# Performance work log

Hardware: AMD Instinct MI355X
Metric: run time of the kernel (lower is better)

Reference implementation:

```python
import jax, jax.numpy as jnp
import numpy as np

T, B, IN, H, OUT = 16384, 1, 32, 512, 1


def setup_inputs() -> dict:
    key = jax.random.key(0)
    ks = jax.random.split(key, 7)
    s = 0.05
    return {
        "input_seq": jax.random.normal(ks[0], (T, B, IN), dtype=jnp.float32),
        "W_ih": jax.random.normal(ks[1], (4 * H, IN), dtype=jnp.float32) * s,
        "W_hh": jax.random.normal(ks[2], (4 * H, H), dtype=jnp.float32) * s,
        "b_ih": jax.random.normal(ks[3], (4 * H,), dtype=jnp.float32) * s,
        "b_hh": jax.random.normal(ks[4], (4 * H,), dtype=jnp.float32) * s,
        "W_lin": jax.random.normal(ks[5], (OUT, H), dtype=jnp.float32) * s,
        "b_lin": jax.random.normal(ks[6], (OUT,), dtype=jnp.float32) * s,
    }


def reference(input_seq, W_ih, W_hh, b_ih, b_hh, W_lin, b_lin):
    # input_seq: [T, 1, IN]; batch=1 as hardcoded by the module's hidden_cell.
    t = input_seq.shape[0]
    x = input_seq.reshape(t, -1)  # [T, IN]
    h_dim = W_hh.shape[1]
    # Precompute input contribution to gates for all timesteps (one big GEMM).
    x_gates = x @ W_ih.T + (b_ih + b_hh)  # [T, 4H]

    def step(carry, xg):
        h, c = carry
        g = xg + W_hh @ h  # [4H]; PyTorch gate order: i, f, g, o
        i = jax.nn.sigmoid(g[:h_dim])
        f = jax.nn.sigmoid(g[h_dim:2 * h_dim])
        gg = jnp.tanh(g[2 * h_dim:3 * h_dim])
        o = jax.nn.sigmoid(g[3 * h_dim:])
        c_new = f * c + i * gg
        h_new = o * jnp.tanh(c_new)
        return (h_new, c_new), h_new

    h0 = jnp.zeros((h_dim,), dtype=input_seq.dtype)
    c0 = jnp.zeros((h_dim,), dtype=input_seq.dtype)
    _, lstm_out = jax.lax.scan(step, (h0, c0), x_gates)  # [T, H]
    predictions = lstm_out @ W_lin.T + b_lin  # [T, OUT]
    return predictions[-1]  # [OUT]
```

## Files before the change

### kernel.cpp

```cpp
#include <hip/hip_runtime.h>
#include <hip/hip_fp16.h>
#include <math.h>


#define T_STEPS 16384
#define IN_DIM  32
#define H_DIM   512
#define SLOTS   32
#define H_SLICE 16
#define KTOT    544
#define CHUNK   136

typedef unsigned int uint32x4 __attribute__((ext_vector_type(4)));

__device__ __forceinline__ float fast_sigmoid(float v) {
  return 1.0f / (1.0f + __expf(-v));
}
__device__ __forceinline__ float fast_tanh(float v) {
  return 2.0f / (1.0f + __expf(-2.0f * v)) - 1.0f;
}

__device__ __forceinline__ void store_pkt(unsigned int* p, unsigned int v) {
  asm volatile("global_store_dword %0, %1, off sc0 sc1"
               :: "v"(p), "v"(v) : "memory");
}
__device__ __forceinline__ uint32x4 load_pkt4(const unsigned int* p) {
  uint32x4 r;
  asm volatile("global_load_dwordx4 %0, %1, off sc0 sc1\n\ts_waitcnt vmcnt(0)"
               : "=&v"(r) : "v"(p) : "memory");
  return r;
}

__launch_bounds__(256, 1)
__global__ void lstm_scan_kernel(
    const float* __restrict__ x,
    const float* __restrict__ Wih,
    const float* __restrict__ Whh,
    const float* __restrict__ bih,
    const float* __restrict__ bhh,
    const float* __restrict__ Wlin,
    const float* __restrict__ blin,
    float* __restrict__ out,
    unsigned int* pub)
{
  const int slot = blockIdx.x;
  const int tid  = threadIdx.x;
  const int w    = tid >> 6;
  const int l    = tid & 63;

  __shared__ __align__(16) float hshm[KTOT];
  __shared__ float red[256];

  const int R = (l >> 4) * H_DIM + slot * H_SLICE + (l & 15);

  float wreg[CHUNK];
  #pragma unroll
  for (int j = 0; j < CHUNK; ++j) {
    const int k = w * CHUNK + j;
    wreg[j] = (k < H_DIM) ? Whh[R * H_DIM + k]
                          : Wih[R * IN_DIM + (k - H_DIM)];
  }
  #pragma unroll
  for (int j = 0; j < CHUNK; ++j)
    asm volatile("v_mov_b32 %0, %0" : "+v"(wreg[j]));

  const float bias = (w == 0) ? (bih[R] + bhh[R]) : 0.0f;

  float c = 0.0f;

  const bool poller = (tid < 128) && ((tid >> 2) != slot);
  if (tid < H_SLICE) hshm[slot * H_SLICE + tid] = 0.0f;

  for (int t = 0; t < T_STEPS; ++t) {
    float xv = (tid < IN_DIM) ? x[t * IN_DIM + tid] : 0.0f;

    if (poller) {
      const unsigned int* p = pub + (t & 1) * H_DIM + tid * 4;
      const unsigned int tg = (unsigned int)t & 0xFFFFu;
      uint32x4 r;
      for (;;) {
        r = load_pkt4(p);
        if ((r.x >> 16) == tg && (r.y >> 16) == tg &&
            (r.z >> 16) == tg && (r.w >> 16) == tg) break;
      }
      float4 hv4;
      hv4.x = __half2float(__ushort_as_half((unsigned short)(r.x & 0xFFFFu)));
      hv4.y = __half2float(__ushort_as_half((unsigned short)(r.y & 0xFFFFu)));
      hv4.z = __half2float(__ushort_as_half((unsigned short)(r.z & 0xFFFFu)));
      hv4.w = __half2float(__ushort_as_half((unsigned short)(r.w & 0xFFFFu)));
      *(float4*)(hshm + tid * 4) = hv4;
    }
    if (tid < IN_DIM) hshm[H_DIM + tid] = xv;
    __syncthreads();

    const float4* hv = (const float4*)(hshm + w * CHUNK);
    float a0 = 0.f, a1 = 0.f, a2 = 0.f, a3 = 0.f;
    #pragma unroll
    for (int q = 0; q < CHUNK / 4; ++q) {
      const float4 h4 = hv[q];
      a0 = fmaf(wreg[4 * q + 0], h4.x, a0);
      a1 = fmaf(wreg[4 * q + 1], h4.y, a1);
      a2 = fmaf(wreg[4 * q + 2], h4.z, a2);
      a3 = fmaf(wreg[4 * q + 3], h4.w, a3);
    }
    red[w * 64 + l] = (a0 + a1) + (a2 + a3);
    __syncthreads();

    if (w == 0) {
      const float g = bias + red[l] + red[64 + l] + red[128 + l] + red[192 + l];
      const float act = (l < 32 || l >= 48) ? fast_sigmoid(g) : fast_tanh(g);
      const int j = l & 15;
      const float ig = __shfl(act, j, 64);
      const float fg = __shfl(act, j + 16, 64);
      const float gt = __shfl(act, j + 32, 64);
      const float og = __shfl(act, j + 48, 64);
      if (l < H_SLICE) {
        c = fg * c + ig * gt;
        const float h = og * fast_tanh(c);
        hshm[slot * H_SLICE + l] = h;
        const unsigned int pkt =
            (((unsigned int)(t + 1) & 0xFFFFu) << 16) |
            (unsigned int)__half_as_ushort(__float2half_rn(h));
        store_pkt(pub + ((t + 1) & 1) * H_DIM + slot * H_SLICE + l, pkt);
      }
    }
  }

  if (slot == 0) {
    if (poller) {
      const unsigned int* p = pub + (T_STEPS & 1) * H_DIM + tid * 4;
      const unsigned int tg = (unsigned int)T_STEPS & 0xFFFFu;
      uint32x4 r;
      for (;;) {
        r = load_pkt4(p);
        if ((r.x >> 16) == tg && (r.y >> 16) == tg &&
            (r.z >> 16) == tg && (r.w >> 16) == tg) break;
      }
      float4 hv4;
      hv4.x = __half2float(__ushort_as_half((unsigned short)(r.x & 0xFFFFu)));
      hv4.y = __half2float(__ushort_as_half((unsigned short)(r.y & 0xFFFFu)));
      hv4.z = __half2float(__ushort_as_half((unsigned short)(r.z & 0xFFFFu)));
      hv4.w = __half2float(__ushort_as_half((unsigned short)(r.w & 0xFFFFu)));
      *(float4*)(hshm + tid * 4) = hv4;
    }
    __syncthreads();
    red[tid] = hshm[2 * tid] * Wlin[2 * tid] +
               hshm[2 * tid + 1] * Wlin[2 * tid + 1];
    __syncthreads();
    if (w == 0) {
      float s = red[l] + red[64 + l] + red[128 + l] + red[192 + l];
      #pragma unroll
      for (int off = 32; off > 0; off >>= 1) s += __shfl_down(s, off, 64);
      if (l == 0) out[0] = s + blin[0];
    }
  }
}

extern "C" void kernel_launch(void* const* d_in, const int* in_sizes, int n_in,
                              void* d_out, int out_size, void* d_ws, size_t ws_size,
                              hipStream_t stream) {
  const float* x    = (const float*)d_in[0];
  const float* Wih  = (const float*)d_in[1];
  const float* Whh  = (const float*)d_in[2];
  const float* bih  = (const float*)d_in[3];
  const float* bhh  = (const float*)d_in[4];
  const float* Wlin = (const float*)d_in[5];
  const float* blin = (const float*)d_in[6];
  float* out = (float*)d_out;

  unsigned int* pub = (unsigned int*)d_ws;

  hipMemsetAsync(d_ws, 0, 4096, stream);
  hipLaunchKernelGGL(lstm_scan_kernel, dim3(SLOTS), dim3(256), 0, stream,
                     x, Wih, Whh, bih, bhh, Wlin, blin, out, pub);
}
```

Measured before the change: 28.60 ms.

## Assign one gate per wave and reduce K-partials with cross-lane shuffles

Each of the four waves now owns one LSTM gate for the block's 16 hidden units. Lanes within a wave split the 544-long K dimension into quarters and combine their partials with xor shuffles, instead of writing every partial to shared memory for wave 0 to sum. All waves then apply their gate activation in parallel and exchange results through a small shared buffer. Every wave updates the cell state redundantly, and the global packet stores are spread across waves. The intent is to shorten the serial reduce-and-activate tail of each timestep, at the cost of duplicated cell arithmetic and more shuffle instructions.

```diff
diff --git a/kernel.cpp b/kernel.cpp
--- a/kernel.cpp
+++ b/kernel.cpp
@@ -9,9 +9,9 @@
 #define SLOTS   32
 #define H_SLICE 16
 #define KTOT    544
-#define CHUNK   136
+#define QCHUNK  136
 
-typedef unsigned int uint32x4 __attribute__((ext_vector_type(4)));
+typedef unsigned int uint4v __attribute__((ext_vector_type(4)));
 
 __device__ __forceinline__ float fast_sigmoid(float v) {
   return 1.0f / (1.0f + __expf(-v));
@@ -24,11 +24,15 @@
   asm volatile("global_store_dword %0, %1, off sc0 sc1"
                :: "v"(p), "v"(v) : "memory");
 }
-__device__ __forceinline__ uint32x4 load_pkt4(const unsigned int* p) {
-  uint32x4 r;
+__device__ __forceinline__ uint4v load_pkt4(const unsigned int* p) {
+  uint4v r;
   asm volatile("global_load_dwordx4 %0, %1, off sc0 sc1\n\ts_waitcnt vmcnt(0)"
                : "=&v"(r) : "v"(p) : "memory");
   return r;
+}
+
+__device__ __forceinline__ float h16(unsigned int lo16) {
+  return __half2float(__ushort_as_half((unsigned short)(lo16 & 0xFFFFu)));
 }
 
 __launch_bounds__(256, 1)
@@ -47,24 +51,27 @@
   const int tid  = threadIdx.x;
   const int w    = tid >> 6;
   const int l    = tid & 63;
+  const int q    = l >> 4;
+  const int j    = l & 15;
 
   __shared__ __align__(16) float hshm[KTOT];
+  __shared__ __align__(16) float actsh[64];
   __shared__ float red[256];
 
-  const int R = (l >> 4) * H_DIM + slot * H_SLICE + (l & 15);
+  const int R = w * H_DIM + slot * H_SLICE + j;
 
-  float wreg[CHUNK];
+  float wreg[QCHUNK];
   #pragma unroll
-  for (int j = 0; j < CHUNK; ++j) {
-    const int k = w * CHUNK + j;
-    wreg[j] = (k < H_DIM) ? Whh[R * H_DIM + k]
+  for (int i = 0; i < QCHUNK; ++i) {
+    const int k = q * QCHUNK + i;
+    wreg[i] = (k < H_DIM) ? Whh[R * H_DIM + k]
                           : Wih[R * IN_DIM + (k - H_DIM)];
   }
   #pragma unroll
-  for (int j = 0; j < CHUNK; ++j)
-    asm volatile("v_mov_b32 %0, %0" : "+v"(wreg[j]));
+  for (int i = 0; i < QCHUNK; ++i)
+    asm volatile("v_mov_b32 %0, %0" : "+v"(wreg[i]));
 
-  const float bias = (w == 0) ? (bih[R] + bhh[R]) : 0.0f;
+  const float bias = bih[R] + bhh[R];
 
   float c = 0.0f;
 
@@ -76,50 +83,46 @@
 
     if (poller) {
       const unsigned int* p = pub + (t & 1) * H_DIM + tid * 4;
-      const unsigned int tg = (unsigned int)t & 0xFFFFu;
-      uint32x4 r;
+      const unsigned int tg = (unsigned int)t;
+      uint4v r;
       for (;;) {
         r = load_pkt4(p);
         if ((r.x >> 16) == tg && (r.y >> 16) == tg &&
             (r.z >> 16) == tg && (r.w >> 16) == tg) break;
       }
       float4 hv4;
-      hv4.x = __half2float(__ushort_as_half((unsigned short)(r.x & 0xFFFFu)));
-      hv4.y = __half2float(__ushort_as_half((unsigned short)(r.y & 0xFFFFu)));
-      hv4.z = __half2float(__ushort_as_half((unsigned short)(r.z & 0xFFFFu)));
-      hv4.w = __half2float(__ushort_as_half((unsigned short)(r.w & 0xFFFFu)));
+      hv4.x = h16(r.x); hv4.y = h16(r.y); hv4.z = h16(r.z); hv4.w = h16(r.w);
       *(float4*)(hshm + tid * 4) = hv4;
     }
     if (tid < IN_DIM) hshm[H_DIM + tid] = xv;
     __syncthreads();
 
-    const float4* hv = (const float4*)(hshm + w * CHUNK);
+    const float4* hv = (const float4*)(hshm + q * QCHUNK);
     float a0 = 0.f, a1 = 0.f, a2 = 0.f, a3 = 0.f;
     #pragma unroll
-    for (int q = 0; q < CHUNK / 4; ++q) {
-      const float4 h4 = hv[q];
-      a0 = fmaf(wreg[4 * q + 0], h4.x, a0);
-      a1 = fmaf(wreg[4 * q + 1], h4.y, a1);
-      a2 = fmaf(wreg[4 * q + 2], h4.z, a2);
-      a3 = fmaf(wreg[4 * q + 3], h4.w, a3);
+    for (int i = 0; i < QCHUNK / 4; ++i) {
+      const float4 h4 = hv[i];
+      a0 = fmaf(wreg[4 * i + 0], h4.x, a0);
+      a1 = fmaf(wreg[4 * i + 1], h4.y, a1);
+      a2 = fmaf(wreg[4 * i + 2], h4.z, a2);
+      a3 = fmaf(wreg[4 * i + 3], h4.w, a3);
     }
-    red[w * 64 + l] = (a0 + a1) + (a2 + a3);
+    float acc = (a0 + a1) + (a2 + a3);
+    acc += __shfl_xor(acc, 16, 64);
+    acc += __shfl_xor(acc, 32, 64);
+    const float g = acc + bias;
+    const float act = (w == 2) ? fast_tanh(g) : fast_sigmoid(g);
+    if (l < 16) actsh[l * 4 + w] = act;
     __syncthreads();
 
-    if (w == 0) {
-      const float g = bias + red[l] + red[64 + l] + red[128 + l] + red[192 + l];
-      const float act = (l < 32 || l >= 48) ? fast_sigmoid(g) : fast_tanh(g);
-      const int j = l & 15;
-      const float ig = __shfl(act, j, 64);
-      const float fg = __shfl(act, j + 16, 64);
-      const float gt = __shfl(act, j + 32, 64);
-      const float og = __shfl(act, j + 48, 64);
-      if (l < H_SLICE) {
-        c = fg * c + ig * gt;
-        const float h = og * fast_tanh(c);
-        hshm[slot * H_SLICE + l] = h;
+    if (l < 16) {
+      const float4 a4 = *(const float4*)(actsh + l * 4);
+      c = a4.y * c + a4.x * a4.z;
+      const float h = a4.w * fast_tanh(c);
+      if (w == 0) hshm[slot * H_SLICE + l] = h;
+      if ((l >> 2) == w) {
         const unsigned int pkt =
-            (((unsigned int)(t + 1) & 0xFFFFu) << 16) |
+            ((unsigned int)(t + 1) << 16) |
             (unsigned int)__half_as_ushort(__float2half_rn(h));
         store_pkt(pub + ((t + 1) & 1) * H_DIM + slot * H_SLICE + l, pkt);
       }
@@ -129,18 +132,15 @@
   if (slot == 0) {
     if (poller) {
       const unsigned int* p = pub + (T_STEPS & 1) * H_DIM + tid * 4;
-      const unsigned int tg = (unsigned int)T_STEPS & 0xFFFFu;
-      uint32x4 r;
+      const unsigned int tg = (unsigned int)T_STEPS;
+      uint4v r;
       for (;;) {
         r = load_pkt4(p);
         if ((r.x >> 16) == tg && (r.y >> 16) == tg &&
             (r.z >> 16) == tg && (r.w >> 16) == tg) break;
       }
       float4 hv4;
-      hv4.x = __half2float(__ushort_as_half((unsigned short)(r.x & 0xFFFFu)));
-      hv4.y = __half2float(__ushort_as_half((unsigned short)(r.y & 0xFFFFu)));
-      hv4.z = __half2float(__ushort_as_half((unsigned short)(r.z & 0xFFFFu)));
-      hv4.w = __half2float(__ushort_as_half((unsigned short)(r.w & 0xFFFFu)));
+      hv4.x = h16(r.x); hv4.y = h16(r.y); hv4.z = h16(r.z); hv4.w = h16(r.w);
       *(float4*)(hshm + tid * 4) = hv4;
     }
     __syncthreads();
```

New measurement: 35.21 ms. +23.1%, slower.
